# Kernel tuning notes

Hardware: AMD Instinct MI355X
Metric: run time of the kernel (lower is better)

The kernel has to match this reference:

```python
import jax, jax.numpy as jnp
import numpy as np

N, M, E = 500000, 125000, 2000000
C_IN, C_OUT = 32, 64


def setup_inputs() -> dict:
    key = jax.random.key(0)
    ks = jax.random.split(key, 8)
    point_bxyz = jax.random.normal(ks[0], (N, 4), dtype=jnp.float32)
    point_feat = jax.random.normal(ks[1], (N, C_IN), dtype=jnp.float32)
    sample_idx = jax.random.randint(ks[2], (M,), 0, N, dtype=jnp.int64 if jax.config.jax_enable_x64 else jnp.int32)
    e_point = jax.random.randint(ks[3], (E,), 0, N, dtype=jnp.int32)
    e_new = jax.random.randint(ks[4], (E,), 0, M, dtype=jnp.int32)
    W1 = jax.random.normal(ks[5], (C_IN + 3, C_OUT), dtype=jnp.float32) * (1.0 / np.sqrt(C_IN + 3))
    b1 = jnp.zeros((C_OUT,), dtype=jnp.float32)
    W2 = jax.random.normal(ks[6], (C_OUT, C_OUT), dtype=jnp.float32) * (1.0 / np.sqrt(C_OUT))
    b2 = jnp.zeros((C_OUT,), dtype=jnp.float32)
    return {"point_bxyz": point_bxyz, "point_feat": point_feat, "sample_idx": sample_idx,
            "e_point": e_point, "e_new": e_new, "W1": W1, "b1": b1, "W2": W2, "b2": b2}


def reference(point_bxyz, point_feat, sample_idx, e_point, e_new, W1, b1, W2, b2):
    # sampler: select M points (FPS modeled as precomputed sample indices)
    new_bxyz = point_bxyz[sample_idx]                          # [M, 4]
    # graph conv: gather per-edge features + relative position (xyz only, col 0 is batch idx)
    rel = point_bxyz[e_point, 1:4] - new_bxyz[e_new, 1:4]      # [E, 3]
    edge_feat = jnp.concatenate([point_feat[e_point], rel], axis=-1)  # [E, C_in+3]
    # per-edge MLP
    h = jax.nn.relu(edge_feat @ W1 + b1)                       # [E, C_out]
    h = jax.nn.relu(h @ W2 + b2)                               # [E, C_out]
    # scatter-max aggregation onto sampled points
    agg = jax.ops.segment_max(h, e_new, num_segments=new_bxyz.shape[0])  # [M, C_out]
    new_feat = jnp.where(jnp.isfinite(agg), agg, 0.0)          # isolated nodes -> 0
    return new_bxyz, new_feat
```

## Files before the change

kernel.cpp:

```cpp
#include <hip/hip_runtime.h>
#include <hip/hip_bf16.h>

#define CIN 32
#define COUT 64
#define SCHUNK 1024
#define T_TILES 8

typedef __attribute__((ext_vector_type(8))) short bf16x8;
typedef __attribute__((ext_vector_type(4))) float f32x4;

__device__ inline short bf16r(float x) {
    unsigned u = __float_as_uint(x);
    return (short)((u + 0x7FFFu + ((u >> 16) & 1u)) >> 16);
}

__device__ inline unsigned pk2(float lo, float hi) {
    __hip_bfloat162 t = __float22bfloat162_rn(make_float2(lo, hi));
    return *(unsigned*)&t;
}

__global__ void prep_kernel(const int4* __restrict__ e_new4,
                            int* __restrict__ mat, int E16, int nbkt,
                            const float* __restrict__ W1,
                            const float* __restrict__ W2,
                            short* __restrict__ wpack,
                            const float4* __restrict__ bxyz4,
                            const int* __restrict__ sidx,
                            float4* __restrict__ out_bxyz,
                            const float* __restrict__ feat,
                            uint4* __restrict__ featb,
                            uint2* __restrict__ pbb,
                            int M, int N, int nbp, int B1, int nbm) {
    __shared__ int h[512];
    int b = blockIdx.x, tid = threadIdx.x;
    if (b < nbp) {
        int p = b * 256 + tid;
        if (p < N) {
            const float4* s = (const float4*)(feat + (size_t)p * CIN);
            float4 f0 = s[0], f1 = s[1], f2 = s[2], f3 = s[3];
            float4 f4 = s[4], f5 = s[5], f6 = s[6], f7 = s[7];
            uint4* d = featb + (size_t)p * 4;
            d[0] = make_uint4(pk2(f0.x, f0.y), pk2(f0.z, f0.w), pk2(f1.x, f1.y), pk2(f1.z, f1.w));
            d[1] = make_uint4(pk2(f2.x, f2.y), pk2(f2.z, f2.w), pk2(f3.x, f3.y), pk2(f3.z, f3.w));
            d[2] = make_uint4(pk2(f4.x, f4.y), pk2(f4.z, f4.w), pk2(f5.x, f5.y), pk2(f5.z, f5.w));
            d[3] = make_uint4(pk2(f6.x, f6.y), pk2(f6.z, f6.w), pk2(f7.x, f7.y), pk2(f7.z, f7.w));
            float4 pb = bxyz4[p];
            pbb[p] = make_uint2(pk2(pb.y, pb.z), pk2(pb.w, 0.f));
        }
    } else if (b < nbp + B1) {
        int blk = b - nbp;
        h[tid] = 0; h[tid + 256] = 0;
        __syncthreads();
        int i = blk * 256 + tid;
        if (i < E16) {
            int4 n0 = e_new4[i * 4 + 0];
            int4 n1 = e_new4[i * 4 + 1];
            int4 n2 = e_new4[i * 4 + 2];
            int4 n3 = e_new4[i * 4 + 3];
            atomicAdd(&h[n0.x >> 8], 1); atomicAdd(&h[n0.y >> 8], 1);
            atomicAdd(&h[n0.z >> 8], 1); atomicAdd(&h[n0.w >> 8], 1);
            atomicAdd(&h[n1.x >> 8], 1); atomicAdd(&h[n1.y >> 8], 1);
            atomicAdd(&h[n1.z >> 8], 1); atomicAdd(&h[n1.w >> 8], 1);
            atomicAdd(&h[n2.x >> 8], 1); atomicAdd(&h[n2.y >> 8], 1);
            atomicAdd(&h[n2.z >> 8], 1); atomicAdd(&h[n2.w >> 8], 1);
            atomicAdd(&h[n3.x >> 8], 1); atomicAdd(&h[n3.y >> 8], 1);
            atomicAdd(&h[n3.z >> 8], 1); atomicAdd(&h[n3.w >> 8], 1);
        }
        __syncthreads();
        if (tid < nbkt)       mat[(size_t)blk * nbkt + tid] = h[tid];
        if (tid + 256 < nbkt) mat[(size_t)blk * nbkt + tid + 256] = h[tid + 256];
    } else if (b < nbp + B1 + nbm) {
        int i = (b - nbp - B1) * 256 + tid;
        if (i < M) out_bxyz[i] = bxyz4[sidx[i]];
    } else {
        int t = (b - nbp - B1 - nbm) * 256 + tid;
        int e = t & 7, l = (t >> 3) & 63, f = t >> 9;
        int g = l >> 4, n16 = l & 15;
        int kc = (f & 7) >> 2, nt = f & 3;
        int k = kc * 32 + g * 8 + e;
        int n = nt * 16 + n16;
        float v;
        if (f < 8) v = (k < CIN + 3) ? W1[k * COUT + n] : 0.f;
        else       v = W2[k * COUT + n];
        wpack[t] = bf16r(v);
    }
}

__global__ void p1s1_kernel(int* __restrict__ mat, int* __restrict__ total,
                            int B1, int nbkt) {
    __shared__ int lds[256];
    int k = blockIdx.x, t = threadIdx.x;
    int i0 = 2 * t, i1 = 2 * t + 1;
    int x0 = (i0 < B1) ? mat[(size_t)i0 * nbkt + k] : 0;
    int x1 = (i1 < B1) ? mat[(size_t)i1 * nbkt + k] : 0;
    int s = x0 + x1;
    int val = s;
    lds[t] = val; __syncthreads();
    for (int off = 1; off < 256; off <<= 1) {
        int x = (t >= off) ? lds[t - off] : 0;
        __syncthreads();
        val += x; lds[t] = val;
        __syncthreads();
    }
    int ex = val - s;
    if (i0 < B1) mat[(size_t)i0 * nbkt + k] = ex;
    if (i1 < B1) mat[(size_t)i1 * nbkt + k] = ex + x0;
    if (t == 255) total[k] = val;
}

__global__ void p1s2_kernel(const int* __restrict__ total,
                            int* __restrict__ base, int nbkt) {
    __shared__ int lds[256];
    int t = threadIdx.x;
    int i0 = 2 * t, i1 = 2 * t + 1;
    int x0 = (i0 < nbkt) ? total[i0] : 0;
    int x1 = (i1 < nbkt) ? total[i1] : 0;
    int s = x0 + x1;
    int val = s;
    lds[t] = val; __syncthreads();
    for (int off = 1; off < 256; off <<= 1) {
        int x = (t >= off) ? lds[t - off] : 0;
        __syncthreads();
        val += x; lds[t] = val;
        __syncthreads();
    }
    int ex = val - s;
    if (i0 < nbkt) base[i0] = ex;
    if (i1 < nbkt) base[i1] = ex + x0;
    if (t == 255) base[nbkt] = val;
}

__global__ void p1c_kernel(const int4* __restrict__ e_new4,
                           const int4* __restrict__ e_pt4,
                           const int* __restrict__ mat,
                           const int* __restrict__ base,
                           uint2* __restrict__ rec, int E16, int nbkt) {
    __shared__ int cur[512];
    int blk = blockIdx.x, tid = threadIdx.x;
    if (tid < nbkt)       cur[tid]       = base[tid]       + mat[(size_t)blk * nbkt + tid];
    if (tid + 256 < nbkt) cur[tid + 256] = base[tid + 256] + mat[(size_t)blk * nbkt + tid + 256];
    __syncthreads();
    int i = blk * 256 + tid;
    if (i >= E16) return;
    int4 n0 = e_new4[i * 4 + 0], n1 = e_new4[i * 4 + 1];
    int4 n2 = e_new4[i * 4 + 2], n3 = e_new4[i * 4 + 3];
    int4 p0 = e_pt4[i * 4 + 0],  p1 = e_pt4[i * 4 + 1];
    int4 p2 = e_pt4[i * 4 + 2],  p3 = e_pt4[i * 4 + 3];
    int sg[16] = {n0.x, n0.y, n0.z, n0.w, n1.x, n1.y, n1.z, n1.w,
                  n2.x, n2.y, n2.z, n2.w, n3.x, n3.y, n3.z, n3.w};
    int ep[16] = {p0.x, p0.y, p0.z, p0.w, p1.x, p1.y, p1.z, p1.w,
                  p2.x, p2.y, p2.z, p2.w, p3.x, p3.y, p3.z, p3.w};
#pragma unroll
    for (int k = 0; k < 16; ++k) {
        int pos = atomicAdd(&cur[sg[k] >> 8], 1);
        rec[pos] = make_uint2((unsigned)sg[k], (unsigned)ep[k]);
    }
}

__global__ void p2a_kernel(const uint2* __restrict__ rec,
                           const int* __restrict__ base,
                           int* __restrict__ counts, int M) {
    __shared__ int h[256];
    int k = blockIdx.x, t = threadIdx.x;
    h[t] = 0; __syncthreads();
    int st = base[k], en = base[k + 1];
    for (int j = st + t; j < en; j += 256)
        atomicAdd(&h[rec[j].x & 255], 1);
    __syncthreads();
    int s = k * 256 + t;
    if (s < M) counts[s] = h[t];
}

__global__ void scanA_kernel(const int* __restrict__ counts,
                             int* __restrict__ row1,
                             int* __restrict__ sums, int M) {
    __shared__ int lds[256];
    int t = threadIdx.x, blk = blockIdx.x;
    int bse = blk * SCHUNK + t * 4;
    int v0 = (bse + 0 < M) ? (counts[bse + 0] + 15) >> 4 : 0;
    int v1 = (bse + 1 < M) ? (counts[bse + 1] + 15) >> 4 : 0;
    int v2 = (bse + 2 < M) ? (counts[bse + 2] + 15) >> 4 : 0;
    int v3 = (bse + 3 < M) ? (counts[bse + 3] + 15) >> 4 : 0;
    int s = v0 + v1 + v2 + v3;
    int val = s;
    lds[t] = val; __syncthreads();
    for (int off = 1; off < 256; off <<= 1) {
        int x = (t >= off) ? lds[t - off] : 0;
        __syncthreads();
        val += x; lds[t] = val;
        __syncthreads();
    }
    int ex = val - s;
    if (bse + 0 < M) row1[bse + 0] = ex + v0;
    if (bse + 1 < M) row1[bse + 1] = ex + v0 + v1;
    if (bse + 2 < M) row1[bse + 2] = ex + v0 + v1 + v2;
    if (bse + 3 < M) row1[bse + 3] = ex + s;
    if (t == 255) sums[blk] = val;
}

__global__ void scanC_kernel(int* __restrict__ row1,
                             const int* __restrict__ sums,
                             int* __restrict__ tstart, int M) {
    __shared__ int lds[256];
    int blk = blockIdx.x, t = threadIdx.x;
    lds[t] = (t < blk) ? sums[t] : 0;
    __syncthreads();
    for (int off = 128; off > 0; off >>= 1) {
        if (t < off) lds[t] += lds[t + off];
        __syncthreads();
    }
    int off0 = lds[0];
    if (blk == 0 && t == 0) tstart[0] = 0;
    int bse = blk * SCHUNK + t * 4;
#pragma unroll
    for (int i = 0; i < 4; ++i)
        if (bse + i < M) row1[bse + i] += off0;
}

__global__ void p2b_kernel(const uint2* __restrict__ rec,
                           const int* __restrict__ base,
                           const int* __restrict__ tstart,
                           int* __restrict__ csr_ep,
                           int* __restrict__ tile_seg, int M) {
    __shared__ int cur[256];
    int k = blockIdx.x, t = threadIdx.x;
    cur[t] = 0; __syncthreads();
    int st = base[k], en = base[k + 1];
    for (int j = st + t; j < en; j += 256) {
        uint2 r = rec[j];
        int s = (int)r.x;
        int tk = atomicAdd(&cur[s & 255], 1);
        csr_ep[(size_t)tstart[s] * 16 + tk] = (int)r.y;
    }
    __syncthreads();
    int s = k * 256 + t;
    if (s < M) {
        int cnt = cur[t];
        if (cnt) {
            int tst = tstart[s];
            int ntl = (cnt + 15) >> 4;
            int prow = tst * 16;
            int ep0 = csr_ep[prow];
            for (int j = cnt; j < ntl * 16; ++j) csr_ep[prow + j] = ep0;
            for (int j = 0; j < ntl; ++j) tile_seg[tst + j] = s;
        }
    }
}

__global__ __launch_bounds__(256)
void agg_kernel(const uint4* __restrict__ featb,
                const uint2* __restrict__ pbb,
                const int* __restrict__ csr_ep,
                const int* __restrict__ tile_seg,
                const int* __restrict__ ntiles_ptr,
                const bf16x8* __restrict__ wpack,
                const float* __restrict__ b1,
                const float* __restrict__ b2,
                const float* __restrict__ W1,
                const float4* __restrict__ new_bxyz4,
                float* __restrict__ out_feat) {
    __shared__ char   h1buf[4][4096];
    __shared__ bf16x8 w2lds[512];

    const int ntiles = ntiles_ptr[0];
    if (blockIdx.x * 4 * T_TILES >= ntiles) return;

    w2lds[threadIdx.x]       = wpack[512 + threadIdx.x];
    w2lds[threadIdx.x + 256] = wpack[768 + threadIdx.x];
    __syncthreads();

    const int lane = threadIdx.x & 63;
    const int w    = threadIdx.x >> 6;
    const int m    = lane & 15;
    const int g    = lane >> 4;

    int wid = blockIdx.x * 4 + w;
    int t0  = wid * T_TILES;
    int niter = min(T_TILES, ntiles - t0);
    if (niter <= 0) return;

    bf16x8 w1b[8];
#pragma unroll
    for (int f = 0; f < 8; ++f) w1b[f] = wpack[f * 64 + lane];

    float b1v[4], b2v[4], w1r0[4], w1r1[4], w1r2[4];
#pragma unroll
    for (int nt = 0; nt < 4; ++nt) {
        int col = nt * 16 + m;
        b1v[nt]  = b1[col];
        b2v[nt]  = b2[col];
        w1r0[nt] = W1[32 * COUT + col];
        w1r1[nt] = W1[33 * COUT + col];
        w1r2[nt] = W1[34 * COUT + col];
    }

    char* h1p = h1buf[w];
    int wA[8];
#pragma unroll
    for (int q = 0; q < 4; ++q) {
        int row = g * 4 + q;
        int kk = (row & 7) << 4;
        wA[q * 2 + 0] = (row * 256 + m * 4) ^ kk;
        wA[q * 2 + 1] = (row * 256 + (m + 16) * 4) ^ kk;
    }
    const int frm = (m & 7) << 4;
    const int rb0 = (m * 256 + g * 32) ^ frm;
    const int rb1 = (m * 256 + g * 32 + 16) ^ frm;

    int* outI = (int*)out_feat;

    int seg0, seg1;
    bf16x8 a10, a11;
    unsigned c4x0, c4y0, c4x1, c4y1;
    float be0[4], be1[4];

#define LOADSLOT(S, TI)                                                       \
    do {                                                                      \
        int ti_ = min((TI), ntiles - 1);                                      \
        seg##S = tile_seg[ti_];                                               \
        unsigned ep_ = (unsigned)csr_ep[ti_ * 16 + m];                        \
        uint2 c_ = pbb[ep_];                                                  \
        c4x##S = c_.x; c4y##S = c_.y;                                         \
        a1##S = ((const bf16x8*)featb)[(size_t)ep_ * 4 + g];                  \
        float4 nb_ = new_bxyz4[seg##S];                                       \
        _Pragma("unroll")                                                     \
        for (int nt = 0; nt < 4; ++nt)                                        \
            be##S[nt] = b1v[nt] - nb_.y * w1r0[nt] - nb_.z * w1r1[nt]         \
                                 - nb_.w * w1r2[nt];                          \
    } while (0)

#define COMPUTE(S)                                                            \
    do {                                                                      \
        bf16x8 a2 = {0, 0, 0, 0, 0, 0, 0, 0};                                 \
        if (g == 0) {                                                         \
            a2[0] = (short)(c4x##S & 0xffffu);                                \
            a2[1] = (short)(c4x##S >> 16);                                    \
            a2[2] = (short)(c4y##S & 0xffffu);                                \
        }                                                                     \
        _Pragma("unroll")                                                     \
        for (int nt = 0; nt < 4; ++nt) {                                      \
            float be = be##S[nt];                                             \
            f32x4 cc = {be, be, be, be};                                      \
            cc = __builtin_amdgcn_mfma_f32_16x16x32_bf16(a1##S, w1b[nt], cc, 0, 0, 0); \
            cc = __builtin_amdgcn_mfma_f32_16x16x32_bf16(a2, w1b[4 + nt], cc, 0, 0, 0); \
            _Pragma("unroll")                                                 \
            for (int q = 0; q < 4; ++q)                                       \
                *(float*)(h1p + wA[q * 2 + (nt & 1)] + (nt >> 1) * 128) =     \
                    fmaxf(cc[q], 0.f);                                        \
        }                                                                     \
        float4 q0 = *(const float4*)(h1p + rb0);                              \
        float4 q1 = *(const float4*)(h1p + rb1);                              \
        float4 q2 = *(const float4*)(h1p + rb0 + 128);                        \
        float4 q3 = *(const float4*)(h1p + rb1 + 128);                        \
        union { bf16x8 v; unsigned u[4]; } A30, A31;                          \
        A30.u[0] = pk2(q0.x, q0.y); A30.u[1] = pk2(q0.z, q0.w);               \
        A30.u[2] = pk2(q1.x, q1.y); A30.u[3] = pk2(q1.z, q1.w);               \
        A31.u[0] = pk2(q2.x, q2.y); A31.u[1] = pk2(q2.z, q2.w);               \
        A31.u[2] = pk2(q3.x, q3.y); A31.u[3] = pk2(q3.z, q3.w);               \
        float vmax[4];                                                        \
        _Pragma("unroll")                                                     \
        for (int nt = 0; nt < 4; ++nt) {                                      \
            bf16x8 wf0 = w2lds[nt * 64 + lane];                               \
            bf16x8 wf1 = w2lds[(4 + nt) * 64 + lane];                         \
            f32x4 cc = {b2v[nt], b2v[nt], b2v[nt], b2v[nt]};                  \
            cc = __builtin_amdgcn_mfma_f32_16x16x32_bf16(A30.v, wf0, cc, 0, 0, 0); \
            cc = __builtin_amdgcn_mfma_f32_16x16x32_bf16(A31.v, wf1, cc, 0, 0, 0); \
            vmax[nt] = fmaxf(fmaxf(cc[0], cc[1]), fmaxf(cc[2], cc[3]));       \
        }                                                                     \
        _Pragma("unroll")                                                     \
        for (int nt = 0; nt < 4; ++nt) {                                      \
            float v = vmax[nt];                                               \
            v = fmaxf(v, __shfl_xor(v, 16));                                  \
            v = fmaxf(v, __shfl_xor(v, 32));                                  \
            vmax[nt] = v;                                                     \
        }                                                                     \
        float outv = (g == 0) ? vmax[0] : (g == 1) ? vmax[1]                  \
                   : (g == 2) ? vmax[2] : vmax[3];                            \
        outv = fmaxf(outv, 0.f);                                              \
        atomicMax(&outI[(size_t)seg##S * COUT + lane], __float_as_int(outv)); \
    } while (0)

    LOADSLOT(0, t0);
    int i = 0;
    for (;;) {
        if (i >= niter) break;
        LOADSLOT(1, t0 + i + 1);
        COMPUTE(0); ++i;
        if (i >= niter) break;
        LOADSLOT(0, t0 + i + 1);
        COMPUTE(1); ++i;
    }
#undef LOADSLOT
#undef COMPUTE
}

extern "C" void kernel_launch(void* const* d_in, const int* in_sizes, int n_in,
                              void* d_out, int out_size, void* d_ws, size_t ws_size,
                              hipStream_t stream) {
    const float* bxyz   = (const float*)d_in[0];
    const float* feat   = (const float*)d_in[1];
    const int*   sidx   = (const int*)d_in[2];
    const int*   e_pt   = (const int*)d_in[3];
    const int*   e_new  = (const int*)d_in[4];
    const float* W1     = (const float*)d_in[5];
    const float* b1     = (const float*)d_in[6];
    const float* W2     = (const float*)d_in[7];
    const float* b2     = (const float*)d_in[8];

    const int N = in_sizes[0] / 4;
    const int M = in_sizes[2];
    const int E = in_sizes[3];

    float* out_bxyz = (float*)d_out;
    float* out_feat = out_bxyz + (size_t)M * 4;

    const int E16  = E / 16;
    const int nbkt = (M + 255) >> 8;
    const int B1   = (E16 + 255) / 256;
    const int nbm  = (M + 255) / 256;
    const int nbp  = (N + 255) / 256;
    const int nchunks = (M + SCHUNK - 1) / SCHUNK;

    char* ws = (char*)d_ws;
    size_t off = 16384;
    size_t o_mat = off;  off += ((size_t)B1 * nbkt * 4 + 63) & ~(size_t)63;
    size_t o_tot = off;  off += ((size_t)nbkt * 4 + 63) & ~(size_t)63;
    size_t o_bas = off;  off += ((size_t)(nbkt + 1) * 4 + 63) & ~(size_t)63;
    size_t o_cnt = off;  off += ((size_t)M * 4 + 63) & ~(size_t)63;
    size_t o_ts  = off;  off += (((size_t)M + 4) * 4 + 63) & ~(size_t)63;
    size_t o_sum = off;  off += 1024;
    size_t o_rec = off;  off += (size_t)E * 8;
    size_t csr_cap = (size_t)E + 15 * (size_t)M + 64;
    size_t o_csr = off;  off += csr_cap * 4;
    size_t o_tsg = off;  off += (csr_cap / 16 + 64) * 4;
    off = (off + 63) & ~(size_t)63;
    size_t o_pbb = off;  off += (size_t)N * 8;
    off = (off + 63) & ~(size_t)63;
    size_t o_fb  = off;  off += (size_t)N * 64;

    short* wpack    = (short*)ws;
    int*   mat      = (int*)(ws + o_mat);
    int*   total    = (int*)(ws + o_tot);
    int*   base     = (int*)(ws + o_bas);
    int*   counts   = (int*)(ws + o_cnt);
    int*   tstart   = (int*)(ws + o_ts);
    int*   sums     = (int*)(ws + o_sum);
    uint2* rec      = (uint2*)(ws + o_rec);
    int*   csr_ep   = (int*)(ws + o_csr);
    int*   tile_seg = (int*)(ws + o_tsg);
    uint2* pbb      = (uint2*)(ws + o_pbb);
    uint4* featb    = (uint4*)(ws + o_fb);
    int*   row1     = tstart + 1;

    hipMemsetAsync(out_feat, 0, (size_t)M * COUT * 4, stream);

    prep_kernel<<<nbp + B1 + nbm + 32, 256, 0, stream>>>(
        (const int4*)e_new, mat, E16, nbkt,
        W1, W2, wpack, (const float4*)bxyz, sidx, (float4*)out_bxyz,
        feat, featb, pbb, M, N, nbp, B1, nbm);

    p1s1_kernel<<<nbkt, 256, 0, stream>>>(mat, total, B1, nbkt);
    p1s2_kernel<<<1, 256, 0, stream>>>(total, base, nbkt);
    p1c_kernel<<<B1, 256, 0, stream>>>(
        (const int4*)e_new, (const int4*)e_pt, mat, base, rec, E16, nbkt);

    p2a_kernel<<<nbkt, 256, 0, stream>>>(rec, base, counts, M);
    scanA_kernel<<<nchunks, 256, 0, stream>>>(counts, row1, sums, M);
    scanC_kernel<<<nchunks, 256, 0, stream>>>(row1, sums, tstart, M);
    p2b_kernel<<<nbkt, 256, 0, stream>>>(rec, base, tstart, csr_ep, tile_seg, M);

    int maxtiles = E / 16 + M;
    int nblocks  = (maxtiles + 4 * T_TILES - 1) / (4 * T_TILES);
    agg_kernel<<<nblocks, 256, 0, stream>>>(
        featb, pbb, csr_ep, tile_seg, tstart + M, (const bf16x8*)wpack,
        b1, b2, W1, (const float4*)out_bxyz, out_feat);
}
```

Baseline: 185.2 us.

## Replace padded per-segment tiles with dense sorted edge stream and run-boundary atomics

Measured after the change: 357.8 us. +93.2%, slower.

```diff
diff --git a/kernel.cpp b/kernel.cpp
--- a/kernel.cpp
+++ b/kernel.cpp
@@ -177,10 +177,10 @@
     __shared__ int lds[256];
     int t = threadIdx.x, blk = blockIdx.x;
     int bse = blk * SCHUNK + t * 4;
-    int v0 = (bse + 0 < M) ? (counts[bse + 0] + 15) >> 4 : 0;
-    int v1 = (bse + 1 < M) ? (counts[bse + 1] + 15) >> 4 : 0;
-    int v2 = (bse + 2 < M) ? (counts[bse + 2] + 15) >> 4 : 0;
-    int v3 = (bse + 3 < M) ? (counts[bse + 3] + 15) >> 4 : 0;
+    int v0 = (bse + 0 < M) ? counts[bse + 0] : 0;
+    int v1 = (bse + 1 < M) ? counts[bse + 1] : 0;
+    int v2 = (bse + 2 < M) ? counts[bse + 2] : 0;
+    int v3 = (bse + 3 < M) ? counts[bse + 3] : 0;
     int s = v0 + v1 + v2 + v3;
     int val = s;
     lds[t] = val; __syncthreads();
@@ -200,7 +200,7 @@
 
 __global__ void scanC_kernel(int* __restrict__ row1,
                              const int* __restrict__ sums,
-                             int* __restrict__ tstart, int M) {
+                             int* __restrict__ row_start, int M) {
     __shared__ int lds[256];
     int blk = blockIdx.x, t = threadIdx.x;
     lds[t] = (t < blk) ? sums[t] : 0;
@@ -210,7 +210,7 @@
         __syncthreads();
     }
     int off0 = lds[0];
-    if (blk == 0 && t == 0) tstart[0] = 0;
+    if (blk == 0 && t == 0) row_start[0] = 0;
     int bse = blk * SCHUNK + t * 4;
 #pragma unroll
     for (int i = 0; i < 4; ++i)
@@ -219,9 +219,8 @@
 
 __global__ void p2b_kernel(const uint2* __restrict__ rec,
                            const int* __restrict__ base,
-                           const int* __restrict__ tstart,
-                           int* __restrict__ csr_ep,
-                           int* __restrict__ tile_seg, int M) {
+                           const int* __restrict__ row_start,
+                           uint2* __restrict__ rec2) {
     __shared__ int cur[256];
     int k = blockIdx.x, t = threadIdx.x;
     cur[t] = 0; __syncthreads();
@@ -230,39 +229,23 @@
         uint2 r = rec[j];
         int s = (int)r.x;
         int tk = atomicAdd(&cur[s & 255], 1);
-        csr_ep[(size_t)tstart[s] * 16 + tk] = (int)r.y;
-    }
-    __syncthreads();
-    int s = k * 256 + t;
-    if (s < M) {
-        int cnt = cur[t];
-        if (cnt) {
-            int tst = tstart[s];
-            int ntl = (cnt + 15) >> 4;
-            int prow = tst * 16;
-            int ep0 = csr_ep[prow];
-            for (int j = cnt; j < ntl * 16; ++j) csr_ep[prow + j] = ep0;
-            for (int j = 0; j < ntl; ++j) tile_seg[tst + j] = s;
-        }
+        rec2[(size_t)row_start[s] + tk] = r;
     }
 }
 
 __global__ __launch_bounds__(256)
 void agg_kernel(const uint4* __restrict__ featb,
                 const uint2* __restrict__ pbb,
-                const int* __restrict__ csr_ep,
-                const int* __restrict__ tile_seg,
-                const int* __restrict__ ntiles_ptr,
+                const uint2* __restrict__ rec2,
                 const bf16x8* __restrict__ wpack,
                 const float* __restrict__ b1,
                 const float* __restrict__ b2,
-                const float* __restrict__ W1,
                 const float4* __restrict__ new_bxyz4,
-                float* __restrict__ out_feat) {
+                float* __restrict__ out_feat,
+                int ntiles, int Elim) {
     __shared__ char   h1buf[4][4096];
     __shared__ bf16x8 w2lds[512];
 
-    const int ntiles = ntiles_ptr[0];
     if (blockIdx.x * 4 * T_TILES >= ntiles) return;
 
     w2lds[threadIdx.x]       = wpack[512 + threadIdx.x];
@@ -283,15 +266,12 @@
 #pragma unroll
     for (int f = 0; f < 8; ++f) w1b[f] = wpack[f * 64 + lane];
 
-    float b1v[4], b2v[4], w1r0[4], w1r1[4], w1r2[4];
+    float b1v[4], b2v[4];
 #pragma unroll
     for (int nt = 0; nt < 4; ++nt) {
         int col = nt * 16 + m;
-        b1v[nt]  = b1[col];
-        b2v[nt]  = b2[col];
-        w1r0[nt] = W1[32 * COUT + col];
-        w1r1[nt] = W1[33 * COUT + col];
-        w1r2[nt] = W1[34 * COUT + col];
+        b1v[nt] = b1[col];
+        b2v[nt] = b2[col];
     }
 
     char* h1p = h1buf[w];
@@ -311,35 +291,38 @@
 
     int seg0, seg1;
     bf16x8 a10, a11;
-    unsigned c4x0, c4y0, c4x1, c4y1;
-    float be0[4], be1[4];
+    unsigned ax0, ay0, ax1, ay1;
 
 #define LOADSLOT(S, TI)                                                       \
     do {                                                                      \
-        int ti_ = min((TI), ntiles - 1);                                      \
-        seg##S = tile_seg[ti_];                                               \
-        unsigned ep_ = (unsigned)csr_ep[ti_ * 16 + m];                        \
-        uint2 c_ = pbb[ep_];                                                  \
-        c4x##S = c_.x; c4y##S = c_.y;                                         \
+        int idx_ = min((TI) * 16 + m, Elim);                                  \
+        uint2 r_ = rec2[idx_];                                                \
+        seg##S = (int)r_.x;                                                   \
+        unsigned ep_ = r_.y;                                                  \
         a1##S = ((const bf16x8*)featb)[(size_t)ep_ * 4 + g];                  \
-        float4 nb_ = new_bxyz4[seg##S];                                       \
-        _Pragma("unroll")                                                     \
-        for (int nt = 0; nt < 4; ++nt)                                        \
-            be##S[nt] = b1v[nt] - nb_.y * w1r0[nt] - nb_.z * w1r1[nt]         \
-                                 - nb_.w * w1r2[nt];                          \
+        ax##S = 0; ay##S = 0;                                                 \
+        if (g == 0) {                                                         \
+            uint2 pb_ = pbb[ep_];                                             \
+            float4 nb_ = new_bxyz4[seg##S];                                   \
+            float py_ = __uint_as_float(pb_.x << 16);                         \
+            float pz_ = __uint_as_float(pb_.x & 0xffff0000u);                 \
+            float pw_ = __uint_as_float(pb_.y << 16);                         \
+            ax##S = pk2(py_ - nb_.y, pz_ - nb_.z);                            \
+            ay##S = (unsigned)(unsigned short)bf16r(pw_ - nb_.w);             \
+        }                                                                     \
     } while (0)
 
 #define COMPUTE(S)                                                            \
     do {                                                                      \
         bf16x8 a2 = {0, 0, 0, 0, 0, 0, 0, 0};                                 \
         if (g == 0) {                                                         \
-            a2[0] = (short)(c4x##S & 0xffffu);                                \
-            a2[1] = (short)(c4x##S >> 16);                                    \
-            a2[2] = (short)(c4y##S & 0xffffu);                                \
+            a2[0] = (short)(ax##S & 0xffffu);                                 \
+            a2[1] = (short)(ax##S >> 16);                                     \
+            a2[2] = (short)ay##S;                                             \
         }                                                                     \
         _Pragma("unroll")                                                     \
         for (int nt = 0; nt < 4; ++nt) {                                      \
-            float be = be##S[nt];                                             \
+            float be = b1v[nt];                                               \
             f32x4 cc = {be, be, be, be};                                      \
             cc = __builtin_amdgcn_mfma_f32_16x16x32_bf16(a1##S, w1b[nt], cc, 0, 0, 0); \
             cc = __builtin_amdgcn_mfma_f32_16x16x32_bf16(a2, w1b[4 + nt], cc, 0, 0, 0); \
@@ -357,27 +340,33 @@
         A30.u[2] = pk2(q1.x, q1.y); A30.u[3] = pk2(q1.z, q1.w);               \
         A31.u[0] = pk2(q2.x, q2.y); A31.u[1] = pk2(q2.z, q2.w);               \
         A31.u[2] = pk2(q3.x, q3.y); A31.u[3] = pk2(q3.z, q3.w);               \
-        float vmax[4];                                                        \
+        int s0_ = __shfl(seg##S, g * 4 + 0);                                  \
+        int s1_ = __shfl(seg##S, g * 4 + 1);                                  \
+        int s2_ = __shfl(seg##S, g * 4 + 2);                                  \
+        int s3_ = __shfl(seg##S, g * 4 + 3);                                  \
+        bool e01 = (s0_ != s1_), e12 = (s1_ != s2_), e23 = (s2_ != s3_);      \
         _Pragma("unroll")                                                     \
         for (int nt = 0; nt < 4; ++nt) {                                      \
             bf16x8 wf0 = w2lds[nt * 64 + lane];                               \
             bf16x8 wf1 = w2lds[(4 + nt) * 64 + lane];                         \
-            f32x4 cc = {b2v[nt], b2v[nt], b2v[nt], b2v[nt]};                  \
+            float bb = b2v[nt];                                               \
+            f32x4 cc = {bb, bb, bb, bb};                                      \
             cc = __builtin_amdgcn_mfma_f32_16x16x32_bf16(A30.v, wf0, cc, 0, 0, 0); \
             cc = __builtin_amdgcn_mfma_f32_16x16x32_bf16(A31.v, wf1, cc, 0, 0, 0); \
-            vmax[nt] = fmaxf(fmaxf(cc[0], cc[1]), fmaxf(cc[2], cc[3]));       \
+            float r0_ = cc[0];                                                \
+            float r1_ = e01 ? cc[1] : fmaxf(r0_, cc[1]);                      \
+            float r2_ = e12 ? cc[2] : fmaxf(r1_, cc[2]);                      \
+            float r3_ = e23 ? cc[3] : fmaxf(r2_, cc[3]);                      \
+            int c_ = m + 16 * nt;                                             \
+            if (e01) atomicMax(&outI[(size_t)s0_ * COUT + c_],                \
+                               __float_as_int(fmaxf(r0_, 0.f)));              \
+            if (e12) atomicMax(&outI[(size_t)s1_ * COUT + c_],                \
+                               __float_as_int(fmaxf(r1_, 0.f)));              \
+            if (e23) atomicMax(&outI[(size_t)s2_ * COUT + c_],                \
+                               __float_as_int(fmaxf(r2_, 0.f)));              \
+            atomicMax(&outI[(size_t)s3_ * COUT + c_],                         \
+                      __float_as_int(fmaxf(r3_, 0.f)));                       \
         }                                                                     \
-        _Pragma("unroll")                                                     \
-        for (int nt = 0; nt < 4; ++nt) {                                      \
-            float v = vmax[nt];                                               \
-            v = fmaxf(v, __shfl_xor(v, 16));                                  \
-            v = fmaxf(v, __shfl_xor(v, 32));                                  \
-            vmax[nt] = v;                                                     \
-        }                                                                     \
-        float outv = (g == 0) ? vmax[0] : (g == 1) ? vmax[1]                  \
-                   : (g == 2) ? vmax[2] : vmax[3];                            \
-        outv = fmaxf(outv, 0.f);                                              \
-        atomicMax(&outI[(size_t)seg##S * COUT + lane], __float_as_int(outv)); \
     } while (0)
 
     LOADSLOT(0, t0);
@@ -430,27 +419,24 @@
     size_t o_ts  = off;  off += (((size_t)M + 4) * 4 + 63) & ~(size_t)63;
     size_t o_sum = off;  off += 1024;
     size_t o_rec = off;  off += (size_t)E * 8;
-    size_t csr_cap = (size_t)E + 15 * (size_t)M + 64;
-    size_t o_csr = off;  off += csr_cap * 4;
-    size_t o_tsg = off;  off += (csr_cap / 16 + 64) * 4;
+    size_t o_rc2 = off;  off += (size_t)E * 8;
     off = (off + 63) & ~(size_t)63;
     size_t o_pbb = off;  off += (size_t)N * 8;
     off = (off + 63) & ~(size_t)63;
     size_t o_fb  = off;  off += (size_t)N * 64;
 
-    short* wpack    = (short*)ws;
-    int*   mat      = (int*)(ws + o_mat);
-    int*   total    = (int*)(ws + o_tot);
-    int*   base     = (int*)(ws + o_bas);
-    int*   counts   = (int*)(ws + o_cnt);
-    int*   tstart   = (int*)(ws + o_ts);
-    int*   sums     = (int*)(ws + o_sum);
-    uint2* rec      = (uint2*)(ws + o_rec);
-    int*   csr_ep   = (int*)(ws + o_csr);
-    int*   tile_seg = (int*)(ws + o_tsg);
-    uint2* pbb      = (uint2*)(ws + o_pbb);
-    uint4* featb    = (uint4*)(ws + o_fb);
-    int*   row1     = tstart + 1;
+    short* wpack     = (short*)ws;
+    int*   mat       = (int*)(ws + o_mat);
+    int*   total     = (int*)(ws + o_tot);
+    int*   base      = (int*)(ws + o_bas);
+    int*   counts    = (int*)(ws + o_cnt);
+    int*   row_start = (int*)(ws + o_ts);
+    int*   sums      = (int*)(ws + o_sum);
+    uint2* rec       = (uint2*)(ws + o_rec);
+    uint2* rec2      = (uint2*)(ws + o_rc2);
+    uint2* pbb       = (uint2*)(ws + o_pbb);
+    uint4* featb     = (uint4*)(ws + o_fb);
+    int*   row1      = row_start + 1;
 
     hipMemsetAsync(out_feat, 0, (size_t)M * COUT * 4, stream);
 
@@ -466,12 +452,12 @@
 
     p2a_kernel<<<nbkt, 256, 0, stream>>>(rec, base, counts, M);
     scanA_kernel<<<nchunks, 256, 0, stream>>>(counts, row1, sums, M);
-    scanC_kernel<<<nchunks, 256, 0, stream>>>(row1, sums, tstart, M);
-    p2b_kernel<<<nbkt, 256, 0, stream>>>(rec, base, tstart, csr_ep, tile_seg, M);
-
-    int maxtiles = E / 16 + M;
-    int nblocks  = (maxtiles + 4 * T_TILES - 1) / (4 * T_TILES);
+    scanC_kernel<<<nchunks, 256, 0, stream>>>(row1, sums, row_start, M);
+    p2b_kernel<<<nbkt, 256, 0, stream>>>(rec, base, row_start, rec2);
+
+    int ntiles  = (E + 15) / 16;
+    int nblocks = (ntiles + 4 * T_TILES - 1) / (4 * T_TILES);
     agg_kernel<<<nblocks, 256, 0, stream>>>(
-        featb, pbb, csr_ep, tile_seg, tstart + M, (const bf16x8*)wpack,
-        b1, b2, W1, (const float4*)out_bxyz, out_feat);
-}
+        featb, pbb, rec2, (const bf16x8*)wpack,
+        b1, b2, (const float4*)out_bxyz, out_feat, ntiles, E - 1);
+}
```
